# Kernel optimization log

Measured on AMD Instinct MI355X. Metric: run time of the kernel, lower is better.

Reference implementation:

```python
import jax, jax.numpy as jnp
import numpy as np

B, I, H, M, A, R, S, O = 256, 512, 1024, 128, 2048, 4, 3, 512
RS = R * M                      # read_size = num_heads * memory_content_size
P_READ = M + S + 3              # key + shift + (beta, gate, gamma) per read head
P = R * P_READ + (3 * M + S + 3)  # write head adds erase(M) + add(M)


def setup_inputs() -> dict:
    key = jax.random.key(0)
    ks = jax.random.split(key, 16)
    x = jax.random.normal(ks[0], (B, I), dtype=jnp.float32)
    h_prev = 0.1 * jax.random.normal(ks[1], (B, H), dtype=jnp.float32)
    c_prev = 0.1 * jax.random.normal(ks[2], (B, H), dtype=jnp.float32)
    read_w_prev = jax.nn.softmax(jax.random.normal(ks[3], (B, R, A)), axis=-1)
    write_w_prev = jax.nn.softmax(jax.random.normal(ks[4], (B, A)), axis=-1)
    # init_state uses normal(mean=0.5, std=0.2) for memory
    memory_prev = 0.5 + 0.2 * jax.random.normal(ks[5], (B, M, A), dtype=jnp.float32)
    read_vec_prev = 0.1 * jax.random.normal(ks[6], (B, RS), dtype=jnp.float32)
    sc = 0.02
    Wx = sc * jax.random.normal(ks[7], (I + RS, 4 * H), dtype=jnp.float32)
    Wh = sc * jax.random.normal(ks[8], (H, 4 * H), dtype=jnp.float32)
    b_lstm = jnp.zeros((4 * H,), dtype=jnp.float32)
    Wo_h = sc * jax.random.normal(ks[9], (H, O), dtype=jnp.float32)
    bo_h = jnp.zeros((O,), dtype=jnp.float32)
    Wint = sc * jax.random.normal(ks[10], (H, P), dtype=jnp.float32)
    b_int = jnp.zeros((P,), dtype=jnp.float32)
    Wout = sc * jax.random.normal(ks[11], (RS, O), dtype=jnp.float32)
    b_out = jnp.zeros((O,), dtype=jnp.float32)
    return dict(x=x, h_prev=h_prev, c_prev=c_prev, read_w_prev=read_w_prev,
                write_w_prev=write_w_prev, memory_prev=memory_prev,
                read_vec_prev=read_vec_prev, Wx=Wx, Wh=Wh, b_lstm=b_lstm,
                Wo_h=Wo_h, bo_h=bo_h, Wint=Wint, b_int=b_int, Wout=Wout, b_out=b_out)


def _address(k, beta, g, s, gamma, w_prev, mem):
    """NTM/DNC addressing: cosine content sim -> softmax -> gate -> circular shift -> sharpen.
    k: [B,Rh,M], beta/g/gamma: [B,Rh], s: [B,Rh,S], w_prev: [B,Rh,A], mem: [B,M,A] -> w: [B,Rh,A]"""
    eps = 1e-8
    kn = jnp.linalg.norm(k, axis=-1, keepdims=True)          # [B,Rh,1]
    mn = jnp.linalg.norm(mem, axis=1)                        # [B,A]
    sim = jnp.einsum('brm,bma->bra', k, mem) / (kn * mn[:, None, :] + eps)
    w_c = jax.nn.softmax(beta[..., None] * sim, axis=-1)
    w_g = g[..., None] * w_c + (1.0 - g[..., None]) * w_prev
    # circular convolution over S shift offsets centered at 0
    rolled = jnp.stack([jnp.roll(w_g, off, axis=-1) for off in range(-(S // 2), S // 2 + 1)], axis=-1)  # [B,Rh,A,S]
    w_s = jnp.einsum('bras,brs->bra', rolled, s)
    w_pow = (w_s + 1e-12) ** gamma[..., None]
    return w_pow / (jnp.sum(w_pow, axis=-1, keepdims=True) + eps)


def reference(x, h_prev, c_prev, read_w_prev, write_w_prev, memory_prev, read_vec_prev,
              Wx, Wh, b_lstm, Wo_h, bo_h, Wint, b_int, Wout, b_out):
    b = x.shape[0]
    # ---- controller (LSTM over [input, prev read vector]) ----
    z = jnp.concatenate([x, read_vec_prev], axis=-1) @ Wx + h_prev @ Wh + b_lstm
    i_g, f_g, g_g, o_g = jnp.split(z, 4, axis=-1)
    c = jax.nn.sigmoid(f_g) * c_prev + jax.nn.sigmoid(i_g) * jnp.tanh(g_g)
    h = jax.nn.sigmoid(o_g) * jnp.tanh(c)
    output_from_hidden = h @ Wo_h + bo_h
    p = h @ Wint + b_int                                    # interface update_data
    # ---- read heads ----
    pr = p[:, :R * P_READ].reshape(b, R, P_READ)
    k_r = pr[..., :M]
    beta_r = jax.nn.softplus(pr[..., M])
    g_r = jax.nn.sigmoid(pr[..., M + 1])
    gamma_r = 1.0 + jax.nn.softplus(pr[..., M + 2])
    s_r = jax.nn.softmax(pr[..., M + 3:], axis=-1)
    w_read = _address(k_r, beta_r, g_r, s_r, gamma_r, read_w_prev, memory_prev)
    # ---- write head ----
    pw = p[:, R * P_READ:]
    k_w = pw[:, :M]
    beta_w = jax.nn.softplus(pw[:, M])
    g_w = jax.nn.sigmoid(pw[:, M + 1])
    gamma_w = 1.0 + jax.nn.softplus(pw[:, M + 2])
    s_w = jax.nn.softmax(pw[:, M + 3:M + 3 + S], axis=-1)
    erase = jax.nn.sigmoid(pw[:, M + 3 + S:2 * M + 3 + S])
    add = pw[:, 2 * M + 3 + S:]
    w_write = _address(k_w[:, None], beta_w[:, None], g_w[:, None], s_w[:, None],
                       gamma_w[:, None], write_w_prev[:, None], memory_prev)[:, 0]
    # ---- read from PREVIOUS memory (as in DNCCell.forward) ----
    read_vec = jnp.einsum('bma,bra->brm', memory_prev, w_read).reshape(b, RS)
    # ---- erase/add memory edit ----
    memory_new = memory_prev * (1.0 - jnp.einsum('bm,ba->bma', erase, w_write)) \
               + jnp.einsum('bm,ba->bma', add, w_write)
    final_output = output_from_hidden + read_vec @ Wout + b_out
    return final_output, memory_new
```

## Files before the change

kernel.cpp:

```cpp
#include <hip/hip_runtime.h>
#include <math.h>

#define B_ 256
#define I_ 512
#define H_ 1024
#define M_ 128
#define A_ 2048
#define R_ 4
#define S_ 3
#define O_ 512
#define RS_ 512
#define P_ 926
#define PW_OFF 536
#define NP_ 1438
#define SK_ 4

typedef unsigned short ushort_t;
typedef __attribute__((ext_vector_type(8))) short bf16x8;
typedef __attribute__((ext_vector_type(4))) float f32x4;
typedef __attribute__((ext_vector_type(4))) unsigned short u16x4;

__device__ __forceinline__ float sigmoidf_(float x) { return 1.0f / (1.0f + expf(-x)); }
__device__ __forceinline__ float softplusf_(float x) {
    return (x > 20.0f) ? x : log1pf(expf(x));
}
__device__ __forceinline__ ushort_t f2bf(float f) {
    unsigned int u = __float_as_uint(f);
    u = (u + 0x7FFFu + ((u >> 16) & 1u)) >> 16;
    return (ushort_t)u;
}

__device__ __forceinline__ float pval(const float* __restrict__ pp,
                                      const float* __restrict__ b_int,
                                      int b, int col) {
    size_t o = (size_t)b * NP_ + col;
    size_t st = (size_t)B_ * NP_;
    return b_int[col] + pp[o] + pp[o + st] + pp[o + 2 * st] + pp[o + 3 * st];
}

__device__ __forceinline__ float block_sum_(float v, float* red) {
    #pragma unroll
    for (int off = 32; off; off >>= 1) v += __shfl_down(v, off, 64);
    __syncthreads();
    if ((threadIdx.x & 63) == 0) red[threadIdx.x >> 6] = v;
    __syncthreads();
    return red[0] + red[1] + red[2] + red[3];
}
__device__ __forceinline__ float block_max_(float v, float* red) {
    #pragma unroll
    for (int off = 32; off; off >>= 1) v = fmaxf(v, __shfl_down(v, off, 64));
    __syncthreads();
    if ((threadIdx.x & 63) == 0) red[threadIdx.x >> 6] = v;
    __syncthreads();
    return fmaxf(fmaxf(red[0], red[1]), fmaxf(red[2], red[3]));
}

__device__ __forceinline__ void transpose_tile(
    const float* __restrict__ W, ushort_t* __restrict__ WT,
    int K, int N, int ostride, int koff, int bx, int by, float (*tile)[33])
{
    int k0 = by * 32, n0 = bx * 32;
    int tx = threadIdx.x & 31, ty = threadIdx.x >> 5;
    #pragma unroll
    for (int i = 0; i < 4; ++i) {
        int k = ty + i * 8;
        int n = n0 + tx;
        float v = (n < N) ? W[(size_t)(k0 + k) * N + n] : 0.0f;
        tile[tx][k] = v;
    }
    __syncthreads();
    #pragma unroll
    for (int i = 0; i < 4; ++i) {
        int nl = ty + i * 8;
        int n = n0 + nl;
        if (n < N) WT[(size_t)n * ostride + koff + k0 + tx] = f2bf(tile[nl][tx]);
    }
}

__global__ __launch_bounds__(256) void setup_kernel(
    const float* __restrict__ x, const float* __restrict__ rv,
    const float* __restrict__ hp,
    const float* __restrict__ Wx, const float* __restrict__ Wh,
    const float* __restrict__ Wint, const float* __restrict__ Wo_h,
    const float* __restrict__ Wout,
    ushort_t* __restrict__ xin, ushort_t* __restrict__ WxhT,
    ushort_t* __restrict__ WpT, ushort_t* __restrict__ WoutT)
{
    __shared__ float tile[32][33];
    int r = blockIdx.x;
    if (r < 4096) { transpose_tile(Wx, WxhT, 1024, 4096, 2048, 0,    r % 128, r / 128, tile); return; }
    r -= 4096;
    if (r < 4096) { transpose_tile(Wh, WxhT, 1024, 4096, 2048, 1024, r % 128, r / 128, tile); return; }
    r -= 4096;
    if (r < 928)  { transpose_tile(Wint, WpT, 1024, 926, 1024, 0,    r % 29,  r / 29,  tile); return; }
    r -= 928;
    if (r < 512)  { transpose_tile(Wo_h, WpT + (size_t)926 * 1024, 1024, 512, 1024, 0, r % 16, r / 16, tile); return; }
    r -= 512;
    if (r < 256)  { transpose_tile(Wout, WoutT, 512, 512, 512, 0,    r % 16,  r / 16,  tile); return; }
    r -= 256;
    int idx = r * 256 + threadIdx.x;
    int b = idx >> 11, j = idx & 2047;
    float v;
    if (j < 512)       v = x[b * 512 + j];
    else if (j < 1024) v = rv[b * 512 + (j - 512)];
    else               v = hp[b * 1024 + (j - 1024)];
    xin[idx] = f2bf(v);
}

template<bool NALIGN>
__global__ __launch_bounds__(256) void gemm_bf16_k(
    const ushort_t* __restrict__ A, int lda,
    const ushort_t* __restrict__ BT, int ldb,
    float* __restrict__ Cpart,
    int N, int Ks)
{
    __shared__ ushort_t As[64][40];
    __shared__ ushort_t Bs[64][40];
    int tid = threadIdx.x;
    int bm0 = blockIdx.y * 64, bn0 = blockIdx.x * 64;
    int kbeg = blockIdx.z * Ks, kend = kbeg + Ks;
    int srow = tid >> 2;
    int scol = (tid & 3) << 3;
    int wv = tid >> 6, l = tid & 63;
    int wm = (wv & 1) * 32, wn = (wv >> 1) * 32;
    int lane16 = l & 15, quad = l >> 4;

    f32x4 z4 = {0.0f, 0.0f, 0.0f, 0.0f};
    f32x4 acc00 = z4, acc01 = z4, acc10 = z4, acc11 = z4;

    const ushort_t* ap = A + (size_t)(bm0 + srow) * lda + scol;
    bool bvalid = NALIGN || (bn0 + srow) < N;
    const ushort_t* bp = BT + (size_t)(bn0 + srow) * ldb + scol;
    float4 fz = {0.0f, 0.0f, 0.0f, 0.0f};

    for (int k0 = kbeg; k0 < kend; k0 += 32) {
        *(float4*)&As[srow][scol] = *(const float4*)(ap + k0);
        if (bvalid) *(float4*)&Bs[srow][scol] = *(const float4*)(bp + k0);
        else        *(float4*)&Bs[srow][scol] = fz;
        __syncthreads();
        bf16x8 a0 = *(const bf16x8*)&As[wm + lane16][quad * 8];
        bf16x8 a1 = *(const bf16x8*)&As[wm + 16 + lane16][quad * 8];
        bf16x8 b0 = *(const bf16x8*)&Bs[wn + lane16][quad * 8];
        bf16x8 b1 = *(const bf16x8*)&Bs[wn + 16 + lane16][quad * 8];
        acc00 = __builtin_amdgcn_mfma_f32_16x16x32_bf16(a0, b0, acc00, 0, 0, 0);
        acc01 = __builtin_amdgcn_mfma_f32_16x16x32_bf16(a0, b1, acc01, 0, 0, 0);
        acc10 = __builtin_amdgcn_mfma_f32_16x16x32_bf16(a1, b0, acc10, 0, 0, 0);
        acc11 = __builtin_amdgcn_mfma_f32_16x16x32_bf16(a1, b1, acc11, 0, 0, 0);
        __syncthreads();
    }

    float* C = Cpart + (size_t)blockIdx.z * gridDim.y * 64 * N;
    #pragma unroll
    for (int gi = 0; gi < 2; ++gi) {
        #pragma unroll
        for (int gj = 0; gj < 2; ++gj) {
            const f32x4& acc = gi == 0 ? (gj == 0 ? acc00 : acc01)
                                       : (gj == 0 ? acc10 : acc11);
            int col = bn0 + wn + gj * 16 + lane16;
            if (NALIGN || col < N) {
                #pragma unroll
                for (int r2 = 0; r2 < 4; ++r2) {
                    int row = bm0 + wm + gi * 16 + quad * 4 + r2;
                    C[(size_t)row * N + col] = acc[r2];
                }
            }
        }
    }
}

__global__ __launch_bounds__(256) void gates_kernel(
    const float* __restrict__ zpart, const float* __restrict__ b_lstm,
    const float* __restrict__ c_prev, ushort_t* __restrict__ h)
{
    int g = blockIdx.x * 256 + threadIdx.x;
    int b = g >> 8, j = (g & 255) << 2;
    size_t st = (size_t)B_ * 4096;
    size_t zb = (size_t)b * 4096 + j;
    f32x4 zs[4];
    #pragma unroll
    for (int q = 0; q < 4; ++q) {
        size_t o = zb + q * 1024;
        f32x4 v = *(const f32x4*)(zpart + o);
        v += *(const f32x4*)(zpart + o + st);
        v += *(const f32x4*)(zpart + o + 2 * st);
        v += *(const f32x4*)(zpart + o + 3 * st);
        v += *(const f32x4*)(b_lstm + q * 1024 + j);
        zs[q] = v;
    }
    f32x4 cp = *(const f32x4*)(c_prev + (size_t)b * 1024 + j);
    u16x4 hv;
    #pragma unroll
    for (int e = 0; e < 4; ++e) {
        float c = sigmoidf_(zs[1][e]) * cp[e] + sigmoidf_(zs[0][e]) * tanhf(zs[2][e]);
        hv[e] = f2bf(sigmoidf_(zs[3][e]) * tanhf(c));
    }
    *(u16x4*)(h + (size_t)b * 1024 + j) = hv;
}

__global__ __launch_bounds__(256) void sim_kernel(
    const float* __restrict__ mem, const float* __restrict__ pohpart,
    const float* __restrict__ b_int,
    float* __restrict__ dots,
    float* __restrict__ mn)
{
    int b = blockIdx.y;
    int a = blockIdx.x * 256 + threadIdx.x;
    __shared__ float ks[5][M_];
    for (int idx = threadIdx.x; idx < 5 * M_; idx += 256) {
        int h = idx >> 7, m = idx & 127;
        int col = (h < 4) ? h * 134 + m : PW_OFF + m;
        ks[h][m] = pval(pohpart, b_int, b, col);
    }
    __syncthreads();
    const float* mb = mem + (size_t)b * M_ * A_ + a;
    float d0 = 0, d1 = 0, d2 = 0, d3 = 0, d4 = 0, nn = 0;
    #pragma unroll 8
    for (int m = 0; m < M_; ++m) {
        float v = mb[(size_t)m * A_];
        d0 += v * ks[0][m]; d1 += v * ks[1][m]; d2 += v * ks[2][m];
        d3 += v * ks[3][m]; d4 += v * ks[4][m];
        nn += v * v;
    }
    size_t base = (size_t)b * 5 * A_ + a;
    dots[base + 0 * A_] = d0; dots[base + 1 * A_] = d1; dots[base + 2 * A_] = d2;
    dots[base + 3 * A_] = d3; dots[base + 4 * A_] = d4;
    mn[(size_t)b * A_ + a] = sqrtf(nn);
}

__global__ __launch_bounds__(256) void address_kernel(
    const float* __restrict__ pohpart, const float* __restrict__ b_int,
    const float* __restrict__ dots, const float* __restrict__ mn,
    const float* __restrict__ read_w_prev, const float* __restrict__ write_w_prev,
    float* __restrict__ w_read, float* __restrict__ w_write)
{
    int head = blockIdx.x;
    int b = blockIdx.y;
    int t = threadIdx.x;
    __shared__ float wg[A_];
    __shared__ float red[4];

    int pb = (head < 4) ? head * 134 : PW_OFF;
    float beta  = softplusf_(pval(pohpart, b_int, b, pb + 128));
    float g     = sigmoidf_(pval(pohpart, b_int, b, pb + 129));
    float gamma = 1.0f + softplusf_(pval(pohpart, b_int, b, pb + 130));
    float e0 = pval(pohpart, b_int, b, pb + 131);
    float e1 = pval(pohpart, b_int, b, pb + 132);
    float e2 = pval(pohpart, b_int, b, pb + 133);
    float smax = fmaxf(e0, fmaxf(e1, e2));
    float x0 = __expf(e0 - smax), x1 = __expf(e1 - smax), x2 = __expf(e2 - smax);
    float sden = x0 + x1 + x2;
    float s0 = x0 / sden, s1 = x1 / sden, s2 = x2 / sden;

    float kacc = 0.0f;
    if (t < M_) { float kv = pval(pohpart, b_int, b, pb + t); kacc = kv * kv; }
    float kn = sqrtf(block_sum_(kacc, red));

    const float* db = dots + ((size_t)b * 5 + head) * A_;
    const float* mb = mn + (size_t)b * A_;
    float logit[8];
    float lmax = -1e30f;
    #pragma unroll
    for (int i = 0; i < 8; ++i) {
        int a = t + 256 * i;
        float sim = db[a] / (kn * mb[a] + 1e-8f);
        logit[i] = beta * sim;
        lmax = fmaxf(lmax, logit[i]);
    }
    lmax = block_max_(lmax, red);
    float ex[8]; float lsum = 0.0f;
    #pragma unroll
    for (int i = 0; i < 8; ++i) { ex[i] = __expf(logit[i] - lmax); lsum += ex[i]; }
    lsum = block_sum_(lsum, red);
    float inv_lsum = 1.0f / lsum;

    const float* wprev = (head < 4) ? read_w_prev + ((size_t)b * 4 + head) * A_
                                    : write_w_prev + (size_t)b * A_;
    #pragma unroll
    for (int i = 0; i < 8; ++i) {
        int a = t + 256 * i;
        wg[a] = g * (ex[i] * inv_lsum) + (1.0f - g) * wprev[a];
    }
    __syncthreads();
    float wpow[8]; float psum = 0.0f;
    #pragma unroll
    for (int i = 0; i < 8; ++i) {
        int a = t + 256 * i;
        float ws = s0 * wg[(a + 1) & (A_ - 1)] + s1 * wg[a] + s2 * wg[(a + A_ - 1) & (A_ - 1)];
        float wp2 = __expf(gamma * __logf(ws + 1e-12f));
        wpow[i] = wp2; psum += wp2;
    }
    psum = block_sum_(psum, red);
    float inv = 1.0f / (psum + 1e-8f);
    float* wout = (head < 4) ? w_read + ((size_t)b * 4 + head) * A_
                             : w_write + (size_t)b * A_;
    #pragma unroll
    for (int i = 0; i < 8; ++i) wout[t + 256 * i] = wpow[i] * inv;
}

__global__ __launch_bounds__(256) void update_kernel(
    const float* __restrict__ mem, const float* __restrict__ pohpart,
    const float* __restrict__ b_int,
    const float* __restrict__ w_read, const float* __restrict__ w_write,
    float* __restrict__ mem_new,
    ushort_t* __restrict__ read_vec)
{
    int bm = blockIdx.x;
    int b = bm >> 7, m = bm & 127;
    int t = threadIdx.x;
    int wv = t >> 6, l = t & 63;
    float er = sigmoidf_(pval(pohpart, b_int, b, 670 + m));
    float ad = pval(pohpart, b_int, b, 798 + m);
    const f32x4* m4  = (const f32x4*)(mem + ((size_t)b * M_ + m) * A_);
    const f32x4* ww4 = (const f32x4*)(w_write + (size_t)b * A_);
    const f32x4* wr4 = (const f32x4*)(w_read + (size_t)b * 4 * A_);
    f32x4* o4 = (f32x4*)(mem_new + ((size_t)b * M_ + m) * A_);
    float s[4] = {0, 0, 0, 0};
    #pragma unroll
    for (int j = 0; j < 2; ++j) {
        int a4 = wv * 128 + l + 64 * j;
        f32x4 v = m4[a4], w = ww4[a4];
        f32x4 r0 = wr4[a4], r1 = wr4[512 + a4], r2 = wr4[1024 + a4], r3 = wr4[1536 + a4];
        f32x4 ov;
        #pragma unroll
        for (int c = 0; c < 4; ++c) {
            ov[c] = v[c] * (1.0f - er * w[c]) + ad * w[c];
            s[0] += v[c] * r0[c];
            s[1] += v[c] * r1[c];
            s[2] += v[c] * r2[c];
            s[3] += v[c] * r3[c];
        }
        o4[a4] = ov;
    }
    __shared__ float part[4][4];
    #pragma unroll
    for (int r = 0; r < 4; ++r) {
        float v = s[r];
        #pragma unroll
        for (int off = 32; off; off >>= 1) v += __shfl_down(v, off, 64);
        if (l == 0) part[wv][r] = v;
    }
    __syncthreads();
    if (t < 4) {
        float sum = part[0][t] + part[1][t] + part[2][t] + part[3][t];
        read_vec[(size_t)b * RS_ + t * M_ + m] = f2bf(sum);
    }
}

__global__ __launch_bounds__(256) void gemm_final_k(
    const ushort_t* __restrict__ A,
    const ushort_t* __restrict__ BT,
    const float* __restrict__ pohpart,
    const float* __restrict__ bo_h, const float* __restrict__ b_out,
    float* __restrict__ C)
{
    __shared__ ushort_t As[64][40];
    __shared__ ushort_t Bs[64][40];
    int tid = threadIdx.x;
    int bm0 = blockIdx.y * 64, bn0 = blockIdx.x * 64;
    int srow = tid >> 2, scol = (tid & 3) << 3;
    int wv = tid >> 6, l = tid & 63;
    int wm = (wv & 1) * 32, wn = (wv >> 1) * 32;
    int lane16 = l & 15, quad = l >> 4;

    f32x4 z4 = {0.0f, 0.0f, 0.0f, 0.0f};
    f32x4 acc00 = z4, acc01 = z4, acc10 = z4, acc11 = z4;
    const ushort_t* ap = A + (size_t)(bm0 + srow) * 512 + scol;
    const ushort_t* bp = BT + (size_t)(bn0 + srow) * 512 + scol;

    for (int k0 = 0; k0 < 512; k0 += 32) {
        *(float4*)&As[srow][scol] = *(const float4*)(ap + k0);
        *(float4*)&Bs[srow][scol] = *(const float4*)(bp + k0);
        __syncthreads();
        bf16x8 a0 = *(const bf16x8*)&As[wm + lane16][quad * 8];
        bf16x8 a1 = *(const bf16x8*)&As[wm + 16 + lane16][quad * 8];
        bf16x8 b0 = *(const bf16x8*)&Bs[wn + lane16][quad * 8];
        bf16x8 b1 = *(const bf16x8*)&Bs[wn + 16 + lane16][quad * 8];
        acc00 = __builtin_amdgcn_mfma_f32_16x16x32_bf16(a0, b0, acc00, 0, 0, 0);
        acc01 = __builtin_amdgcn_mfma_f32_16x16x32_bf16(a0, b1, acc01, 0, 0, 0);
        acc10 = __builtin_amdgcn_mfma_f32_16x16x32_bf16(a1, b0, acc10, 0, 0, 0);
        acc11 = __builtin_amdgcn_mfma_f32_16x16x32_bf16(a1, b1, acc11, 0, 0, 0);
        __syncthreads();
    }

    size_t st = (size_t)B_ * NP_;
    #pragma unroll
    for (int gi = 0; gi < 2; ++gi) {
        #pragma unroll
        for (int gj = 0; gj < 2; ++gj) {
            const f32x4& acc = gi == 0 ? (gj == 0 ? acc00 : acc01)
                                       : (gj == 0 ? acc10 : acc11);
            int col = bn0 + wn + gj * 16 + lane16;
            float badd = bo_h[col] + b_out[col];
            #pragma unroll
            for (int r2 = 0; r2 < 4; ++r2) {
                int row = bm0 + wm + gi * 16 + quad * 4 + r2;
                size_t o = (size_t)row * NP_ + 926 + col;
                float oh = pohpart[o] + pohpart[o + st] + pohpart[o + 2 * st] + pohpart[o + 3 * st];
                C[(size_t)row * 512 + col] = acc[r2] + badd + oh;
            }
        }
    }
}

extern "C" void kernel_launch(void* const* d_in, const int* in_sizes, int n_in,
                              void* d_out, int out_size, void* d_ws, size_t ws_size,
                              hipStream_t stream) {
    (void)in_sizes; (void)n_in; (void)out_size; (void)ws_size;
    const float* x            = (const float*)d_in[0];
    const float* h_prev       = (const float*)d_in[1];
    const float* c_prev       = (const float*)d_in[2];
    const float* read_w_prev  = (const float*)d_in[3];
    const float* write_w_prev = (const float*)d_in[4];
    const float* memory_prev  = (const float*)d_in[5];
    const float* read_vec_prev= (const float*)d_in[6];
    const float* Wx           = (const float*)d_in[7];
    const float* Wh           = (const float*)d_in[8];
    const float* b_lstm       = (const float*)d_in[9];
    const float* Wo_h         = (const float*)d_in[10];
    const float* bo_h         = (const float*)d_in[11];
    const float* Wint         = (const float*)d_in[12];
    const float* b_int        = (const float*)d_in[13];
    const float* Wout         = (const float*)d_in[14];
    const float* b_out        = (const float*)d_in[15];
    float* out = (float*)d_out;
    float* mem_new_out = out + (size_t)B_ * O_;

    char* wsp = (char*)d_ws;
    ushort_t* xin_bf = (ushort_t*)wsp; wsp += (size_t)B_ * 2048 * 2;
    ushort_t* h_bf   = (ushort_t*)wsp; wsp += (size_t)B_ * H_ * 2;
    ushort_t* rv_bf  = (ushort_t*)wsp; wsp += (size_t)B_ * RS_ * 2;
    ushort_t* WxhT   = (ushort_t*)wsp; wsp += (size_t)4096 * 2048 * 2;
    ushort_t* WpT    = (ushort_t*)wsp; wsp += (size_t)NP_ * 1024 * 2;
    ushort_t* WoutT  = (ushort_t*)wsp; wsp += (size_t)512 * 512 * 2;
    float* zpart     = (float*)wsp;    wsp += (size_t)SK_ * B_ * 4096 * 4;
    float* pohpart   = (float*)wsp;    wsp += (size_t)SK_ * B_ * NP_ * 4;
    float* dots      = (float*)wsp;    wsp += (size_t)B_ * 5 * A_ * 4;
    float* mn        = (float*)wsp;    wsp += (size_t)B_ * A_ * 4;
    float* w_read    = (float*)wsp;    wsp += (size_t)B_ * R_ * A_ * 4;
    float* w_write   = (float*)wsp;    wsp += (size_t)B_ * A_ * 4;

    setup_kernel<<<dim3(4096 + 4096 + 928 + 512 + 256 + 2048), 256, 0, stream>>>(
        x, read_vec_prev, h_prev, Wx, Wh, Wint, Wo_h, Wout,
        xin_bf, WxhT, WpT, WoutT);
    gemm_bf16_k<true><<<dim3(4096 / 64, B_ / 64, SK_), 256, 0, stream>>>(
        xin_bf, 2048, WxhT, 2048, zpart, 4096, 2048 / SK_);
    gates_kernel<<<dim3(B_ * H_ / 1024), 256, 0, stream>>>(zpart, b_lstm, c_prev, h_bf);
    gemm_bf16_k<false><<<dim3(23, B_ / 64, SK_), 256, 0, stream>>>(
        h_bf, 1024, WpT, 1024, pohpart, NP_, 1024 / SK_);
    sim_kernel<<<dim3(A_ / 256, B_), 256, 0, stream>>>(memory_prev, pohpart, b_int, dots, mn);
    address_kernel<<<dim3(5, B_), 256, 0, stream>>>(
        pohpart, b_int, dots, mn, read_w_prev, write_w_prev, w_read, w_write);
    update_kernel<<<dim3(B_ * M_), 256, 0, stream>>>(
        memory_prev, pohpart, b_int, w_read, w_write, mem_new_out, rv_bf);
    gemm_final_k<<<dim3(O_ / 64, B_ / 64), 256, 0, stream>>>(
        rv_bf, WoutT, pohpart, bo_h, b_out, out);
}
```

Measured before the change: 670.9 us.

## Vectorize sim/address kernels and retile memory update to reuse addressing weights

The sim kernel now has each thread handle four adjacent memory columns with float4 loads, and it launches four times fewer blocks. The address kernel switches to float4 loads and stores in a contiguous layout. The update kernel is retiled so each block covers 8 memory rows by half the columns, loading the read and write weights once per block instead of once per row. Read-vector partials are written in fp32 per half and summed and converted to bf16 inside the final GEMM's A-tile load, reusing the xin_bf workspace for the partials. The aims are fewer redundant weight reads and wider memory transactions, at the cost of fewer blocks for the sim kernel and more registers per thread.

```diff
diff --git a/kernel.cpp b/kernel.cpp
--- a/kernel.cpp
+++ b/kernel.cpp
@@ -204,7 +204,7 @@
     float* __restrict__ mn)
 {
     int b = blockIdx.y;
-    int a = blockIdx.x * 256 + threadIdx.x;
+    int a = (blockIdx.x * 256 + threadIdx.x) * 4;
     __shared__ float ks[5][M_];
     for (int idx = threadIdx.x; idx < 5 * M_; idx += 256) {
         int h = idx >> 7, m = idx & 127;
@@ -213,18 +213,43 @@
     }
     __syncthreads();
     const float* mb = mem + (size_t)b * M_ * A_ + a;
-    float d0 = 0, d1 = 0, d2 = 0, d3 = 0, d4 = 0, nn = 0;
-    #pragma unroll 8
-    for (int m = 0; m < M_; ++m) {
-        float v = mb[(size_t)m * A_];
-        d0 += v * ks[0][m]; d1 += v * ks[1][m]; d2 += v * ks[2][m];
-        d3 += v * ks[3][m]; d4 += v * ks[4][m];
-        nn += v * v;
+    f32x4 z = {0.0f, 0.0f, 0.0f, 0.0f};
+    f32x4 d0 = z, d1 = z, d2 = z, d3 = z, d4 = z, nn = z;
+    #pragma unroll 2
+    for (int m = 0; m < M_; m += 4) {
+        f32x4 vv[4];
+        #pragma unroll
+        for (int mm = 0; mm < 4; ++mm)
+            vv[mm] = *(const f32x4*)(mb + (size_t)(m + mm) * A_);
+        f32x4 k0 = *(const f32x4*)&ks[0][m];
+        f32x4 k1 = *(const f32x4*)&ks[1][m];
+        f32x4 k2 = *(const f32x4*)&ks[2][m];
+        f32x4 k3 = *(const f32x4*)&ks[3][m];
+        f32x4 k4 = *(const f32x4*)&ks[4][m];
+        #pragma unroll
+        for (int mm = 0; mm < 4; ++mm) {
+            #pragma unroll
+            for (int c = 0; c < 4; ++c) {
+                float v = vv[mm][c];
+                d0[c] += v * k0[mm];
+                d1[c] += v * k1[mm];
+                d2[c] += v * k2[mm];
+                d3[c] += v * k3[mm];
+                d4[c] += v * k4[mm];
+                nn[c] += v * v;
+            }
+        }
     }
     size_t base = (size_t)b * 5 * A_ + a;
-    dots[base + 0 * A_] = d0; dots[base + 1 * A_] = d1; dots[base + 2 * A_] = d2;
-    dots[base + 3 * A_] = d3; dots[base + 4 * A_] = d4;
-    mn[(size_t)b * A_ + a] = sqrtf(nn);
+    *(f32x4*)(dots + base + 0 * A_) = d0;
+    *(f32x4*)(dots + base + 1 * A_) = d1;
+    *(f32x4*)(dots + base + 2 * A_) = d2;
+    *(f32x4*)(dots + base + 3 * A_) = d3;
+    *(f32x4*)(dots + base + 4 * A_) = d4;
+    f32x4 rt;
+    #pragma unroll
+    for (int c = 0; c < 4; ++c) rt[c] = sqrtf(nn[c]);
+    *(f32x4*)(mn + (size_t)b * A_ + a) = rt;
 }
 
 __global__ __launch_bounds__(256) void address_kernel(
@@ -257,44 +282,63 @@
 
     const float* db = dots + ((size_t)b * 5 + head) * A_;
     const float* mb = mn + (size_t)b * A_;
-    float logit[8];
+    f32x4 dA = *(const f32x4*)(db + 4 * t);
+    f32x4 dB = *(const f32x4*)(db + 1024 + 4 * t);
+    f32x4 mA = *(const f32x4*)(mb + 4 * t);
+    f32x4 mB = *(const f32x4*)(mb + 1024 + 4 * t);
+    f32x4 lA, lB;
     float lmax = -1e30f;
     #pragma unroll
-    for (int i = 0; i < 8; ++i) {
-        int a = t + 256 * i;
-        float sim = db[a] / (kn * mb[a] + 1e-8f);
-        logit[i] = beta * sim;
-        lmax = fmaxf(lmax, logit[i]);
+    for (int c = 0; c < 4; ++c) {
+        lA[c] = beta * dA[c] / (kn * mA[c] + 1e-8f);
+        lB[c] = beta * dB[c] / (kn * mB[c] + 1e-8f);
+        lmax = fmaxf(lmax, fmaxf(lA[c], lB[c]));
     }
     lmax = block_max_(lmax, red);
-    float ex[8]; float lsum = 0.0f;
-    #pragma unroll
-    for (int i = 0; i < 8; ++i) { ex[i] = __expf(logit[i] - lmax); lsum += ex[i]; }
+    f32x4 eA, eB;
+    float lsum = 0.0f;
+    #pragma unroll
+    for (int c = 0; c < 4; ++c) {
+        eA[c] = __expf(lA[c] - lmax);
+        eB[c] = __expf(lB[c] - lmax);
+        lsum += eA[c] + eB[c];
+    }
     lsum = block_sum_(lsum, red);
     float inv_lsum = 1.0f / lsum;
 
     const float* wprev = (head < 4) ? read_w_prev + ((size_t)b * 4 + head) * A_
                                     : write_w_prev + (size_t)b * A_;
-    #pragma unroll
-    for (int i = 0; i < 8; ++i) {
-        int a = t + 256 * i;
-        wg[a] = g * (ex[i] * inv_lsum) + (1.0f - g) * wprev[a];
-    }
-    __syncthreads();
-    float wpow[8]; float psum = 0.0f;
-    #pragma unroll
-    for (int i = 0; i < 8; ++i) {
-        int a = t + 256 * i;
+    f32x4 pA = *(const f32x4*)(wprev + 4 * t);
+    f32x4 pB = *(const f32x4*)(wprev + 1024 + 4 * t);
+    f32x4 gA, gB;
+    #pragma unroll
+    for (int c = 0; c < 4; ++c) {
+        gA[c] = g * (eA[c] * inv_lsum) + (1.0f - g) * pA[c];
+        gB[c] = g * (eB[c] * inv_lsum) + (1.0f - g) * pB[c];
+    }
+    *(f32x4*)&wg[4 * t] = gA;
+    *(f32x4*)&wg[1024 + 4 * t] = gB;
+    __syncthreads();
+    f32x4 wA, wB;
+    float psum = 0.0f;
+    #pragma unroll
+    for (int c = 0; c < 4; ++c) {
+        int a = 4 * t + c;
         float ws = s0 * wg[(a + 1) & (A_ - 1)] + s1 * wg[a] + s2 * wg[(a + A_ - 1) & (A_ - 1)];
-        float wp2 = __expf(gamma * __logf(ws + 1e-12f));
-        wpow[i] = wp2; psum += wp2;
+        wA[c] = __expf(gamma * __logf(ws + 1e-12f));
+        a = 1024 + 4 * t + c;
+        ws = s0 * wg[(a + 1) & (A_ - 1)] + s1 * wg[a] + s2 * wg[(a + A_ - 1) & (A_ - 1)];
+        wB[c] = __expf(gamma * __logf(ws + 1e-12f));
+        psum += wA[c] + wB[c];
     }
     psum = block_sum_(psum, red);
     float inv = 1.0f / (psum + 1e-8f);
+    #pragma unroll
+    for (int c = 0; c < 4; ++c) { wA[c] *= inv; wB[c] *= inv; }
     float* wout = (head < 4) ? w_read + ((size_t)b * 4 + head) * A_
                              : w_write + (size_t)b * A_;
-    #pragma unroll
-    for (int i = 0; i < 8; ++i) wout[t + 256 * i] = wpow[i] * inv;
+    *(f32x4*)(wout + 4 * t) = wA;
+    *(f32x4*)(wout + 1024 + 4 * t) = wB;
 }
 
 __global__ __launch_bounds__(256) void update_kernel(
@@ -302,52 +346,71 @@
     const float* __restrict__ b_int,
     const float* __restrict__ w_read, const float* __restrict__ w_write,
     float* __restrict__ mem_new,
-    ushort_t* __restrict__ read_vec)
-{
-    int bm = blockIdx.x;
-    int b = bm >> 7, m = bm & 127;
+    float* __restrict__ rv_part)
+{
+    int blk = blockIdx.x;
+    int b = blk >> 5;
+    int half = (blk >> 4) & 1;
+    int m0 = (blk & 15) << 3;
     int t = threadIdx.x;
     int wv = t >> 6, l = t & 63;
-    float er = sigmoidf_(pval(pohpart, b_int, b, 670 + m));
-    float ad = pval(pohpart, b_int, b, 798 + m);
-    const f32x4* m4  = (const f32x4*)(mem + ((size_t)b * M_ + m) * A_);
-    const f32x4* ww4 = (const f32x4*)(w_write + (size_t)b * A_);
-    const f32x4* wr4 = (const f32x4*)(w_read + (size_t)b * 4 * A_);
-    f32x4* o4 = (f32x4*)(mem_new + ((size_t)b * M_ + m) * A_);
-    float s[4] = {0, 0, 0, 0};
-    #pragma unroll
-    for (int j = 0; j < 2; ++j) {
-        int a4 = wv * 128 + l + 64 * j;
-        f32x4 v = m4[a4], w = ww4[a4];
-        f32x4 r0 = wr4[a4], r1 = wr4[512 + a4], r2 = wr4[1024 + a4], r3 = wr4[1536 + a4];
+    __shared__ float ser[8], sad[8];
+    __shared__ float spart[4][8][4];
+    if (t < 8)       ser[t] = sigmoidf_(pval(pohpart, b_int, b, 670 + m0 + t));
+    else if (t < 16) sad[t - 8] = pval(pohpart, b_int, b, 798 + m0 + (t - 8));
+
+    int col = half * 1024 + t * 4;
+    const float* wrb = w_read + (size_t)b * 4 * A_ + col;
+    f32x4 ww  = *(const f32x4*)(w_write + (size_t)b * A_ + col);
+    f32x4 wr0 = *(const f32x4*)(wrb);
+    f32x4 wr1 = *(const f32x4*)(wrb + A_);
+    f32x4 wr2 = *(const f32x4*)(wrb + 2 * A_);
+    f32x4 wr3 = *(const f32x4*)(wrb + 3 * A_);
+    __syncthreads();
+
+    float acc[8][4];
+    #pragma unroll
+    for (int mi = 0; mi < 8; ++mi)
+        acc[mi][0] = acc[mi][1] = acc[mi][2] = acc[mi][3] = 0.0f;
+
+    const float* mrow = mem + ((size_t)b * M_ + m0) * A_ + col;
+    float* orow = mem_new + ((size_t)b * M_ + m0) * A_ + col;
+    #pragma unroll
+    for (int mi = 0; mi < 8; ++mi) {
+        f32x4 v = *(const f32x4*)(mrow + (size_t)mi * A_);
+        float er = ser[mi], ad = sad[mi];
         f32x4 ov;
         #pragma unroll
         for (int c = 0; c < 4; ++c) {
-            ov[c] = v[c] * (1.0f - er * w[c]) + ad * w[c];
-            s[0] += v[c] * r0[c];
-            s[1] += v[c] * r1[c];
-            s[2] += v[c] * r2[c];
-            s[3] += v[c] * r3[c];
+            ov[c] = v[c] * (1.0f - er * ww[c]) + ad * ww[c];
+            acc[mi][0] += v[c] * wr0[c];
+            acc[mi][1] += v[c] * wr1[c];
+            acc[mi][2] += v[c] * wr2[c];
+            acc[mi][3] += v[c] * wr3[c];
         }
-        o4[a4] = ov;
-    }
-    __shared__ float part[4][4];
-    #pragma unroll
-    for (int r = 0; r < 4; ++r) {
-        float v = s[r];
-        #pragma unroll
-        for (int off = 32; off; off >>= 1) v += __shfl_down(v, off, 64);
-        if (l == 0) part[wv][r] = v;
-    }
-    __syncthreads();
-    if (t < 4) {
-        float sum = part[0][t] + part[1][t] + part[2][t] + part[3][t];
-        read_vec[(size_t)b * RS_ + t * M_ + m] = f2bf(sum);
+        *(f32x4*)(orow + (size_t)mi * A_) = ov;
+    }
+
+    #pragma unroll
+    for (int mi = 0; mi < 8; ++mi) {
+        #pragma unroll
+        for (int h = 0; h < 4; ++h) {
+            float v = acc[mi][h];
+            #pragma unroll
+            for (int off = 32; off; off >>= 1) v += __shfl_down(v, off, 64);
+            if (l == 0) spart[wv][mi][h] = v;
+        }
+    }
+    __syncthreads();
+    if (t < 32) {
+        int mi = t >> 2, h = t & 3;
+        float s = spart[0][mi][h] + spart[1][mi][h] + spart[2][mi][h] + spart[3][mi][h];
+        rv_part[((size_t)half * B_ + b) * RS_ + h * M_ + m0 + mi] = s;
     }
 }
 
 __global__ __launch_bounds__(256) void gemm_final_k(
-    const ushort_t* __restrict__ A,
+    const float* __restrict__ rv_part,
     const ushort_t* __restrict__ BT,
     const float* __restrict__ pohpart,
     const float* __restrict__ bo_h, const float* __restrict__ b_out,
@@ -364,11 +427,18 @@
 
     f32x4 z4 = {0.0f, 0.0f, 0.0f, 0.0f};
     f32x4 acc00 = z4, acc01 = z4, acc10 = z4, acc11 = z4;
-    const ushort_t* ap = A + (size_t)(bm0 + srow) * 512 + scol;
+    const float* rp0 = rv_part + (size_t)(bm0 + srow) * RS_ + scol;
+    const float* rp1 = rp0 + (size_t)B_ * RS_;
     const ushort_t* bp = BT + (size_t)(bn0 + srow) * 512 + scol;
 
     for (int k0 = 0; k0 < 512; k0 += 32) {
-        *(float4*)&As[srow][scol] = *(const float4*)(ap + k0);
+        f32x4 u0 = *(const f32x4*)(rp0 + k0) + *(const f32x4*)(rp1 + k0);
+        f32x4 u1 = *(const f32x4*)(rp0 + k0 + 4) + *(const f32x4*)(rp1 + k0 + 4);
+        u16x4 w0, w1;
+        #pragma unroll
+        for (int c = 0; c < 4; ++c) { w0[c] = f2bf(u0[c]); w1[c] = f2bf(u1[c]); }
+        *(u16x4*)&As[srow][scol] = w0;
+        *(u16x4*)&As[srow][scol + 4] = w1;
         *(float4*)&Bs[srow][scol] = *(const float4*)(bp + k0);
         __syncthreads();
         bf16x8 a0 = *(const bf16x8*)&As[wm + lane16][quad * 8];
@@ -428,7 +498,6 @@
     char* wsp = (char*)d_ws;
     ushort_t* xin_bf = (ushort_t*)wsp; wsp += (size_t)B_ * 2048 * 2;
     ushort_t* h_bf   = (ushort_t*)wsp; wsp += (size_t)B_ * H_ * 2;
-    ushort_t* rv_bf  = (ushort_t*)wsp; wsp += (size_t)B_ * RS_ * 2;
     ushort_t* WxhT   = (ushort_t*)wsp; wsp += (size_t)4096 * 2048 * 2;
     ushort_t* WpT    = (ushort_t*)wsp; wsp += (size_t)NP_ * 1024 * 2;
     ushort_t* WoutT  = (ushort_t*)wsp; wsp += (size_t)512 * 512 * 2;
@@ -438,6 +507,7 @@
     float* mn        = (float*)wsp;    wsp += (size_t)B_ * A_ * 4;
     float* w_read    = (float*)wsp;    wsp += (size_t)B_ * R_ * A_ * 4;
     float* w_write   = (float*)wsp;    wsp += (size_t)B_ * A_ * 4;
+    float* rv_part   = (float*)xin_bf;
 
     setup_kernel<<<dim3(4096 + 4096 + 928 + 512 + 256 + 2048), 256, 0, stream>>>(
         x, read_vec_prev, h_prev, Wx, Wh, Wint, Wo_h, Wout,
@@ -447,11 +517,11 @@
     gates_kernel<<<dim3(B_ * H_ / 1024), 256, 0, stream>>>(zpart, b_lstm, c_prev, h_bf);
     gemm_bf16_k<false><<<dim3(23, B_ / 64, SK_), 256, 0, stream>>>(
         h_bf, 1024, WpT, 1024, pohpart, NP_, 1024 / SK_);
-    sim_kernel<<<dim3(A_ / 256, B_), 256, 0, stream>>>(memory_prev, pohpart, b_int, dots, mn);
+    sim_kernel<<<dim3(A_ / 1024, B_), 256, 0, stream>>>(memory_prev, pohpart, b_int, dots, mn);
     address_kernel<<<dim3(5, B_), 256, 0, stream>>>(
         pohpart, b_int, dots, mn, read_w_prev, write_w_prev, w_read, w_write);
-    update_kernel<<<dim3(B_ * M_), 256, 0, stream>>>(
-        memory_prev, pohpart, b_int, w_read, w_write, mem_new_out, rv_bf);
+    update_kernel<<<dim3(B_ * 32), 256, 0, stream>>>(
+        memory_prev, pohpart, b_int, w_read, w_write, mem_new_out, rv_part);
     gemm_final_k<<<dim3(O_ / 64, B_ / 64), 256, 0, stream>>>(
-        rv_bf, WoutT, pohpart, bo_h, b_out, out);
-}
+        rv_part, WoutT, pohpart, bo_h, b_out, out);
+}
```

Result: faster. 635.3 us (-5.3%).

## Fuse similarity, addressing, memory update and output GEMM into one per-batch kernel

Applied to the files above, without the earlier changes.

Replaces the sim, address, update and final GEMM kernels with a single kernel that runs one 512-thread block per batch element. Similarity dots, addressing weights and the read vector stay in shared memory, and the output projection becomes an fp32 FMA loop reading Wout directly, so the Wout transpose is dropped. This removes the dots, mn and weight round-trips through global memory plus three launches. In exchange only 256 blocks are launched, memory is read twice per block, and LDS use is large, which may limit occupancy.

```diff
diff --git a/kernel.cpp b/kernel.cpp
--- a/kernel.cpp
+++ b/kernel.cpp
@@ -38,21 +38,23 @@
     return b_int[col] + pp[o] + pp[o + st] + pp[o + 2 * st] + pp[o + 3 * st];
 }
 
-__device__ __forceinline__ float block_sum_(float v, float* red) {
+__device__ __forceinline__ float bsum8(float v, float* red, int wv, int l) {
     #pragma unroll
     for (int off = 32; off; off >>= 1) v += __shfl_down(v, off, 64);
     __syncthreads();
-    if ((threadIdx.x & 63) == 0) red[threadIdx.x >> 6] = v;
-    __syncthreads();
-    return red[0] + red[1] + red[2] + red[3];
-}
-__device__ __forceinline__ float block_max_(float v, float* red) {
+    if (l == 0) red[wv] = v;
+    __syncthreads();
+    return red[0] + red[1] + red[2] + red[3] + red[4] + red[5] + red[6] + red[7];
+}
+__device__ __forceinline__ float bmax8(float v, float* red, int wv, int l) {
     #pragma unroll
     for (int off = 32; off; off >>= 1) v = fmaxf(v, __shfl_down(v, off, 64));
     __syncthreads();
-    if ((threadIdx.x & 63) == 0) red[threadIdx.x >> 6] = v;
-    __syncthreads();
-    return fmaxf(fmaxf(red[0], red[1]), fmaxf(red[2], red[3]));
+    if (l == 0) red[wv] = v;
+    __syncthreads();
+    float m0 = fmaxf(fmaxf(red[0], red[1]), fmaxf(red[2], red[3]));
+    float m1 = fmaxf(fmaxf(red[4], red[5]), fmaxf(red[6], red[7]));
+    return fmaxf(m0, m1);
 }
 
 __device__ __forceinline__ void transpose_tile(
@@ -82,9 +84,8 @@
     const float* __restrict__ hp,
     const float* __restrict__ Wx, const float* __restrict__ Wh,
     const float* __restrict__ Wint, const float* __restrict__ Wo_h,
-    const float* __restrict__ Wout,
     ushort_t* __restrict__ xin, ushort_t* __restrict__ WxhT,
-    ushort_t* __restrict__ WpT, ushort_t* __restrict__ WoutT)
+    ushort_t* __restrict__ WpT)
 {
     __shared__ float tile[32][33];
     int r = blockIdx.x;
@@ -96,8 +97,6 @@
     r -= 928;
     if (r < 512)  { transpose_tile(Wo_h, WpT + (size_t)926 * 1024, 1024, 512, 1024, 0, r % 16, r / 16, tile); return; }
     r -= 512;
-    if (r < 256)  { transpose_tile(Wout, WoutT, 512, 512, 512, 0,    r % 16,  r / 16,  tile); return; }
-    r -= 256;
     int idx = r * 256 + threadIdx.x;
     int b = idx >> 11, j = idx & 2047;
     float v;
@@ -197,208 +196,203 @@
     *(u16x4*)(h + (size_t)b * 1024 + j) = hv;
 }
 
-__global__ __launch_bounds__(256) void sim_kernel(
+__global__ __launch_bounds__(512) void mega_kernel(
     const float* __restrict__ mem, const float* __restrict__ pohpart,
     const float* __restrict__ b_int,
-    float* __restrict__ dots,
-    float* __restrict__ mn)
+    const float* __restrict__ read_w_prev, const float* __restrict__ write_w_prev,
+    const float* __restrict__ Wout, const float* __restrict__ bo_h,
+    const float* __restrict__ b_out,
+    float* __restrict__ out,
+    float* __restrict__ mem_new)
 {
-    int b = blockIdx.y;
-    int a = blockIdx.x * 256 + threadIdx.x;
+    int b = blockIdx.x;
+    int t = threadIdx.x;
+    int wv = t >> 6, l = t & 63;
+
+    __shared__ float dw[5][A_];
+    __shared__ float wg[A_];
     __shared__ float ks[5][M_];
-    for (int idx = threadIdx.x; idx < 5 * M_; idx += 256) {
+    __shared__ float rvp[M_][8][4];
+    __shared__ float red[8];
+
+    for (int idx = t; idx < 5 * M_; idx += 512) {
         int h = idx >> 7, m = idx & 127;
         int col = (h < 4) ? h * 134 + m : PW_OFF + m;
         ks[h][m] = pval(pohpart, b_int, b, col);
     }
     __syncthreads();
-    const float* mb = mem + (size_t)b * M_ * A_ + a;
-    float d0 = 0, d1 = 0, d2 = 0, d3 = 0, d4 = 0, nn = 0;
-    #pragma unroll 8
-    for (int m = 0; m < M_; ++m) {
-        float v = mb[(size_t)m * A_];
-        d0 += v * ks[0][m]; d1 += v * ks[1][m]; d2 += v * ks[2][m];
-        d3 += v * ks[3][m]; d4 += v * ks[4][m];
-        nn += v * v;
-    }
-    size_t base = (size_t)b * 5 * A_ + a;
-    dots[base + 0 * A_] = d0; dots[base + 1 * A_] = d1; dots[base + 2 * A_] = d2;
-    dots[base + 3 * A_] = d3; dots[base + 4 * A_] = d4;
-    mn[(size_t)b * A_ + a] = sqrtf(nn);
-}
-
-__global__ __launch_bounds__(256) void address_kernel(
-    const float* __restrict__ pohpart, const float* __restrict__ b_int,
-    const float* __restrict__ dots, const float* __restrict__ mn,
-    const float* __restrict__ read_w_prev, const float* __restrict__ write_w_prev,
-    float* __restrict__ w_read, float* __restrict__ w_write)
-{
-    int head = blockIdx.x;
-    int b = blockIdx.y;
-    int t = threadIdx.x;
-    __shared__ float wg[A_];
-    __shared__ float red[4];
-
-    int pb = (head < 4) ? head * 134 : PW_OFF;
-    float beta  = softplusf_(pval(pohpart, b_int, b, pb + 128));
-    float g     = sigmoidf_(pval(pohpart, b_int, b, pb + 129));
-    float gamma = 1.0f + softplusf_(pval(pohpart, b_int, b, pb + 130));
-    float e0 = pval(pohpart, b_int, b, pb + 131);
-    float e1 = pval(pohpart, b_int, b, pb + 132);
-    float e2 = pval(pohpart, b_int, b, pb + 133);
-    float smax = fmaxf(e0, fmaxf(e1, e2));
-    float x0 = __expf(e0 - smax), x1 = __expf(e1 - smax), x2 = __expf(e2 - smax);
-    float sden = x0 + x1 + x2;
-    float s0 = x0 / sden, s1 = x1 / sden, s2 = x2 / sden;
-
-    float kacc = 0.0f;
-    if (t < M_) { float kv = pval(pohpart, b_int, b, pb + t); kacc = kv * kv; }
-    float kn = sqrtf(block_sum_(kacc, red));
-
-    const float* db = dots + ((size_t)b * 5 + head) * A_;
-    const float* mb = mn + (size_t)b * A_;
-    float logit[8];
-    float lmax = -1e30f;
-    #pragma unroll
-    for (int i = 0; i < 8; ++i) {
-        int a = t + 256 * i;
-        float sim = db[a] / (kn * mb[a] + 1e-8f);
-        logit[i] = beta * sim;
-        lmax = fmaxf(lmax, logit[i]);
-    }
-    lmax = block_max_(lmax, red);
-    float ex[8]; float lsum = 0.0f;
-    #pragma unroll
-    for (int i = 0; i < 8; ++i) { ex[i] = __expf(logit[i] - lmax); lsum += ex[i]; }
-    lsum = block_sum_(lsum, red);
-    float inv_lsum = 1.0f / lsum;
-
-    const float* wprev = (head < 4) ? read_w_prev + ((size_t)b * 4 + head) * A_
-                                    : write_w_prev + (size_t)b * A_;
-    #pragma unroll
-    for (int i = 0; i < 8; ++i) {
-        int a = t + 256 * i;
-        wg[a] = g * (ex[i] * inv_lsum) + (1.0f - g) * wprev[a];
-    }
-    __syncthreads();
-    float wpow[8]; float psum = 0.0f;
-    #pragma unroll
-    for (int i = 0; i < 8; ++i) {
-        int a = t + 256 * i;
-        float ws = s0 * wg[(a + 1) & (A_ - 1)] + s1 * wg[a] + s2 * wg[(a + A_ - 1) & (A_ - 1)];
-        float wp2 = __expf(gamma * __logf(ws + 1e-12f));
-        wpow[i] = wp2; psum += wp2;
-    }
-    psum = block_sum_(psum, red);
-    float inv = 1.0f / (psum + 1e-8f);
-    float* wout = (head < 4) ? w_read + ((size_t)b * 4 + head) * A_
-                             : w_write + (size_t)b * A_;
-    #pragma unroll
-    for (int i = 0; i < 8; ++i) wout[t + 256 * i] = wpow[i] * inv;
-}
-
-__global__ __launch_bounds__(256) void update_kernel(
-    const float* __restrict__ mem, const float* __restrict__ pohpart,
-    const float* __restrict__ b_int,
-    const float* __restrict__ w_read, const float* __restrict__ w_write,
-    float* __restrict__ mem_new,
-    ushort_t* __restrict__ read_vec)
-{
-    int bm = blockIdx.x;
-    int b = bm >> 7, m = bm & 127;
-    int t = threadIdx.x;
-    int wv = t >> 6, l = t & 63;
-    float er = sigmoidf_(pval(pohpart, b_int, b, 670 + m));
-    float ad = pval(pohpart, b_int, b, 798 + m);
-    const f32x4* m4  = (const f32x4*)(mem + ((size_t)b * M_ + m) * A_);
-    const f32x4* ww4 = (const f32x4*)(w_write + (size_t)b * A_);
-    const f32x4* wr4 = (const f32x4*)(w_read + (size_t)b * 4 * A_);
-    f32x4* o4 = (f32x4*)(mem_new + ((size_t)b * M_ + m) * A_);
-    float s[4] = {0, 0, 0, 0};
-    #pragma unroll
-    for (int j = 0; j < 2; ++j) {
-        int a4 = wv * 128 + l + 64 * j;
-        f32x4 v = m4[a4], w = ww4[a4];
-        f32x4 r0 = wr4[a4], r1 = wr4[512 + a4], r2 = wr4[1024 + a4], r3 = wr4[1536 + a4];
-        f32x4 ov;
+
+    const float* mb = mem + (size_t)b * M_ * A_ + 4 * t;
+    f32x4 z = {0.0f, 0.0f, 0.0f, 0.0f};
+    f32x4 d0 = z, d1 = z, d2 = z, d3 = z, d4 = z, nn = z;
+    #pragma unroll 2
+    for (int m = 0; m < M_; m += 4) {
+        f32x4 vv[4];
+        #pragma unroll
+        for (int mm = 0; mm < 4; ++mm)
+            vv[mm] = *(const f32x4*)(mb + (size_t)(m + mm) * A_);
+        #pragma unroll
+        for (int mm = 0; mm < 4; ++mm) {
+            float k0 = ks[0][m + mm], k1 = ks[1][m + mm], k2 = ks[2][m + mm];
+            float k3 = ks[3][m + mm], k4 = ks[4][m + mm];
+            #pragma unroll
+            for (int c = 0; c < 4; ++c) {
+                float v = vv[mm][c];
+                d0[c] += v * k0; d1[c] += v * k1; d2[c] += v * k2;
+                d3[c] += v * k3; d4[c] += v * k4;
+                nn[c] += v * v;
+            }
+        }
+    }
+    *(f32x4*)&dw[0][4 * t] = d0;
+    *(f32x4*)&dw[1][4 * t] = d1;
+    *(f32x4*)&dw[2][4 * t] = d2;
+    *(f32x4*)&dw[3][4 * t] = d3;
+    *(f32x4*)&dw[4][4 * t] = d4;
+    f32x4 rt;
+    #pragma unroll
+    for (int c = 0; c < 4; ++c) rt[c] = sqrtf(nn[c]);
+
+    for (int head = 0; head < 5; ++head) {
+        int pb = (head < 4) ? head * 134 : PW_OFF;
+        float beta  = softplusf_(pval(pohpart, b_int, b, pb + 128));
+        float g     = sigmoidf_(pval(pohpart, b_int, b, pb + 129));
+        float gamma = 1.0f + softplusf_(pval(pohpart, b_int, b, pb + 130));
+        float e0 = pval(pohpart, b_int, b, pb + 131);
+        float e1 = pval(pohpart, b_int, b, pb + 132);
+        float e2 = pval(pohpart, b_int, b, pb + 133);
+        float smax = fmaxf(e0, fmaxf(e1, e2));
+        float x0 = __expf(e0 - smax), x1 = __expf(e1 - smax), x2 = __expf(e2 - smax);
+        float sden = x0 + x1 + x2;
+        float s0 = x0 / sden, s1 = x1 / sden, s2 = x2 / sden;
+
+        float kacc = (t < M_) ? ks[head][t] * ks[head][t] : 0.0f;
+        float kn = sqrtf(bsum8(kacc, red, wv, l));
+
+        f32x4 dd = *(const f32x4*)&dw[head][4 * t];
+        f32x4 lg;
+        float lmax = -1e30f;
         #pragma unroll
         for (int c = 0; c < 4; ++c) {
-            ov[c] = v[c] * (1.0f - er * w[c]) + ad * w[c];
-            s[0] += v[c] * r0[c];
-            s[1] += v[c] * r1[c];
-            s[2] += v[c] * r2[c];
-            s[3] += v[c] * r3[c];
-        }
-        o4[a4] = ov;
-    }
-    __shared__ float part[4][4];
-    #pragma unroll
-    for (int r = 0; r < 4; ++r) {
-        float v = s[r];
-        #pragma unroll
-        for (int off = 32; off; off >>= 1) v += __shfl_down(v, off, 64);
-        if (l == 0) part[wv][r] = v;
-    }
-    __syncthreads();
-    if (t < 4) {
-        float sum = part[0][t] + part[1][t] + part[2][t] + part[3][t];
-        read_vec[(size_t)b * RS_ + t * M_ + m] = f2bf(sum);
-    }
-}
-
-__global__ __launch_bounds__(256) void gemm_final_k(
-    const ushort_t* __restrict__ A,
-    const ushort_t* __restrict__ BT,
-    const float* __restrict__ pohpart,
-    const float* __restrict__ bo_h, const float* __restrict__ b_out,
-    float* __restrict__ C)
-{
-    __shared__ ushort_t As[64][40];
-    __shared__ ushort_t Bs[64][40];
-    int tid = threadIdx.x;
-    int bm0 = blockIdx.y * 64, bn0 = blockIdx.x * 64;
-    int srow = tid >> 2, scol = (tid & 3) << 3;
-    int wv = tid >> 6, l = tid & 63;
-    int wm = (wv & 1) * 32, wn = (wv >> 1) * 32;
-    int lane16 = l & 15, quad = l >> 4;
-
-    f32x4 z4 = {0.0f, 0.0f, 0.0f, 0.0f};
-    f32x4 acc00 = z4, acc01 = z4, acc10 = z4, acc11 = z4;
-    const ushort_t* ap = A + (size_t)(bm0 + srow) * 512 + scol;
-    const ushort_t* bp = BT + (size_t)(bn0 + srow) * 512 + scol;
-
-    for (int k0 = 0; k0 < 512; k0 += 32) {
-        *(float4*)&As[srow][scol] = *(const float4*)(ap + k0);
-        *(float4*)&Bs[srow][scol] = *(const float4*)(bp + k0);
+            lg[c] = beta * dd[c] / (kn * rt[c] + 1e-8f);
+            lmax = fmaxf(lmax, lg[c]);
+        }
+        lmax = bmax8(lmax, red, wv, l);
+        f32x4 ex;
+        float lsum = 0.0f;
+        #pragma unroll
+        for (int c = 0; c < 4; ++c) { ex[c] = __expf(lg[c] - lmax); lsum += ex[c]; }
+        lsum = bsum8(lsum, red, wv, l);
+        float inv_lsum = 1.0f / lsum;
+
+        const float* wprev = (head < 4) ? read_w_prev + ((size_t)b * 4 + head) * A_
+                                        : write_w_prev + (size_t)b * A_;
+        f32x4 pv = *(const f32x4*)(wprev + 4 * t);
+        f32x4 gv;
+        #pragma unroll
+        for (int c = 0; c < 4; ++c)
+            gv[c] = g * (ex[c] * inv_lsum) + (1.0f - g) * pv[c];
+        *(f32x4*)&wg[4 * t] = gv;
         __syncthreads();
-        bf16x8 a0 = *(const bf16x8*)&As[wm + lane16][quad * 8];
-        bf16x8 a1 = *(const bf16x8*)&As[wm + 16 + lane16][quad * 8];
-        bf16x8 b0 = *(const bf16x8*)&Bs[wn + lane16][quad * 8];
-        bf16x8 b1 = *(const bf16x8*)&Bs[wn + 16 + lane16][quad * 8];
-        acc00 = __builtin_amdgcn_mfma_f32_16x16x32_bf16(a0, b0, acc00, 0, 0, 0);
-        acc01 = __builtin_amdgcn_mfma_f32_16x16x32_bf16(a0, b1, acc01, 0, 0, 0);
-        acc10 = __builtin_amdgcn_mfma_f32_16x16x32_bf16(a1, b0, acc10, 0, 0, 0);
-        acc11 = __builtin_amdgcn_mfma_f32_16x16x32_bf16(a1, b1, acc11, 0, 0, 0);
+        f32x4 wp;
+        float psum = 0.0f;
+        #pragma unroll
+        for (int c = 0; c < 4; ++c) {
+            int a = 4 * t + c;
+            float ws = s0 * wg[(a + 1) & (A_ - 1)] + s1 * wg[a] + s2 * wg[(a + A_ - 1) & (A_ - 1)];
+            wp[c] = __expf(gamma * __logf(ws + 1e-12f));
+            psum += wp[c];
+        }
+        psum = bsum8(psum, red, wv, l);
+        float inv = 1.0f / (psum + 1e-8f);
+        #pragma unroll
+        for (int c = 0; c < 4; ++c) wp[c] *= inv;
+        *(f32x4*)&dw[head][4 * t] = wp;
         __syncthreads();
     }
 
-    size_t st = (size_t)B_ * NP_;
-    #pragma unroll
-    for (int gi = 0; gi < 2; ++gi) {
-        #pragma unroll
-        for (int gj = 0; gj < 2; ++gj) {
-            const f32x4& acc = gi == 0 ? (gj == 0 ? acc00 : acc01)
-                                       : (gj == 0 ? acc10 : acc11);
-            int col = bn0 + wn + gj * 16 + lane16;
-            float badd = bo_h[col] + b_out[col];
+    float* er_s = &ks[0][0];
+    float* ad_s = &ks[1][0];
+    if (t < M_)            er_s[t] = sigmoidf_(pval(pohpart, b_int, b, 670 + t));
+    else if (t < 2 * M_)   ad_s[t - M_] = pval(pohpart, b_int, b, 798 + (t - M_));
+    __syncthreads();
+
+    f32x4 ww = *(const f32x4*)&dw[4][4 * t];
+    f32x4 w0 = *(const f32x4*)&dw[0][4 * t];
+    f32x4 w1 = *(const f32x4*)&dw[1][4 * t];
+    f32x4 w2 = *(const f32x4*)&dw[2][4 * t];
+    f32x4 w3 = *(const f32x4*)&dw[3][4 * t];
+    const float* mrow = mem + (size_t)b * M_ * A_ + 4 * t;
+    float* orow = mem_new + (size_t)b * M_ * A_ + 4 * t;
+    #pragma unroll 1
+    for (int m0v = 0; m0v < M_; m0v += 4) {
+        f32x4 vv[4];
+        #pragma unroll
+        for (int mm = 0; mm < 4; ++mm)
+            vv[mm] = *(const f32x4*)(mrow + (size_t)(m0v + mm) * A_);
+        #pragma unroll
+        for (int mm = 0; mm < 4; ++mm) {
+            float er = er_s[m0v + mm], ad = ad_s[m0v + mm];
+            f32x4 ov;
+            float a0 = 0, a1 = 0, a2 = 0, a3 = 0;
             #pragma unroll
-            for (int r2 = 0; r2 < 4; ++r2) {
-                int row = bm0 + wm + gi * 16 + quad * 4 + r2;
-                size_t o = (size_t)row * NP_ + 926 + col;
-                float oh = pohpart[o] + pohpart[o + st] + pohpart[o + 2 * st] + pohpart[o + 3 * st];
-                C[(size_t)row * 512 + col] = acc[r2] + badd + oh;
+            for (int c = 0; c < 4; ++c) {
+                float v = vv[mm][c];
+                ov[c] = v * (1.0f - er * ww[c]) + ad * ww[c];
+                a0 += v * w0[c]; a1 += v * w1[c]; a2 += v * w2[c]; a3 += v * w3[c];
             }
-        }
+            *(f32x4*)(orow + (size_t)(m0v + mm) * A_) = ov;
+            float ah0 = a0, ah1 = a1, ah2 = a2, ah3 = a3;
+            #pragma unroll
+            for (int off = 32; off; off >>= 1) {
+                ah0 += __shfl_down(ah0, off, 64);
+                ah1 += __shfl_down(ah1, off, 64);
+                ah2 += __shfl_down(ah2, off, 64);
+                ah3 += __shfl_down(ah3, off, 64);
+            }
+            if (l == 0) {
+                rvp[m0v + mm][wv][0] = ah0;
+                rvp[m0v + mm][wv][1] = ah1;
+                rvp[m0v + mm][wv][2] = ah2;
+                rvp[m0v + mm][wv][3] = ah3;
+            }
+        }
+    }
+    __syncthreads();
+
+    float* rvs = wg;
+    {
+        int h = t >> 7, m = t & 127;
+        float s = 0.0f;
+        #pragma unroll
+        for (int w8 = 0; w8 < 8; ++w8) s += rvp[m][w8][h];
+        rvs[t] = s;
+    }
+    __syncthreads();
+
+    float* part = &rvp[0][0][0];
+    {
+        int q = t >> 7;
+        int oc = (t & 127) * 4;
+        f32x4 acc = {0.0f, 0.0f, 0.0f, 0.0f};
+        const float* wob = Wout + (size_t)q * M_ * O_ + oc;
+        #pragma unroll 4
+        for (int k = 0; k < M_; ++k) {
+            float rvk = rvs[q * M_ + k];
+            f32x4 wv4 = *(const f32x4*)(wob + (size_t)k * O_);
+            #pragma unroll
+            for (int c = 0; c < 4; ++c) acc[c] += rvk * wv4[c];
+        }
+        *(f32x4*)&part[q * 512 + oc] = acc;
+    }
+    __syncthreads();
+    {
+        int o = t;
+        size_t st = (size_t)B_ * NP_;
+        size_t po = (size_t)b * NP_ + 926 + o;
+        float oh = pohpart[po] + pohpart[po + st] + pohpart[po + 2 * st] + pohpart[po + 3 * st];
+        float s = part[o] + part[512 + o] + part[1024 + o] + part[1536 + o];
+        out[(size_t)b * O_ + o] = s + oh + bo_h[o] + b_out[o];
     }
 }
 
@@ -428,30 +422,20 @@
     char* wsp = (char*)d_ws;
     ushort_t* xin_bf = (ushort_t*)wsp; wsp += (size_t)B_ * 2048 * 2;
     ushort_t* h_bf   = (ushort_t*)wsp; wsp += (size_t)B_ * H_ * 2;
-    ushort_t* rv_bf  = (ushort_t*)wsp; wsp += (size_t)B_ * RS_ * 2;
     ushort_t* WxhT   = (ushort_t*)wsp; wsp += (size_t)4096 * 2048 * 2;
     ushort_t* WpT    = (ushort_t*)wsp; wsp += (size_t)NP_ * 1024 * 2;
-    ushort_t* WoutT  = (ushort_t*)wsp; wsp += (size_t)512 * 512 * 2;
     float* zpart     = (float*)wsp;    wsp += (size_t)SK_ * B_ * 4096 * 4;
     float* pohpart   = (float*)wsp;    wsp += (size_t)SK_ * B_ * NP_ * 4;
-    float* dots      = (float*)wsp;    wsp += (size_t)B_ * 5 * A_ * 4;
-    float* mn        = (float*)wsp;    wsp += (size_t)B_ * A_ * 4;
-    float* w_read    = (float*)wsp;    wsp += (size_t)B_ * R_ * A_ * 4;
-    float* w_write   = (float*)wsp;    wsp += (size_t)B_ * A_ * 4;
-
-    setup_kernel<<<dim3(4096 + 4096 + 928 + 512 + 256 + 2048), 256, 0, stream>>>(
-        x, read_vec_prev, h_prev, Wx, Wh, Wint, Wo_h, Wout,
-        xin_bf, WxhT, WpT, WoutT);
+
+    setup_kernel<<<dim3(4096 + 4096 + 928 + 512 + 2048), 256, 0, stream>>>(
+        x, read_vec_prev, h_prev, Wx, Wh, Wint, Wo_h,
+        xin_bf, WxhT, WpT);
     gemm_bf16_k<true><<<dim3(4096 / 64, B_ / 64, SK_), 256, 0, stream>>>(
         xin_bf, 2048, WxhT, 2048, zpart, 4096, 2048 / SK_);
     gates_kernel<<<dim3(B_ * H_ / 1024), 256, 0, stream>>>(zpart, b_lstm, c_prev, h_bf);
     gemm_bf16_k<false><<<dim3(23, B_ / 64, SK_), 256, 0, stream>>>(
         h_bf, 1024, WpT, 1024, pohpart, NP_, 1024 / SK_);
-    sim_kernel<<<dim3(A_ / 256, B_), 256, 0, stream>>>(memory_prev, pohpart, b_int, dots, mn);
-    address_kernel<<<dim3(5, B_), 256, 0, stream>>>(
-        pohpart, b_int, dots, mn, read_w_prev, write_w_prev, w_read, w_write);
-    update_kernel<<<dim3(B_ * M_), 256, 0, stream>>>(
-        memory_prev, pohpart, b_int, w_read, w_write, mem_new_out, rv_bf);
-    gemm_final_k<<<dim3(O_ / 64, B_ / 64), 256, 0, stream>>>(
-        rv_bf, WoutT, pohpart, bo_h, b_out, out);
-}
+    mega_kernel<<<dim3(B_), 512, 0, stream>>>(
+        memory_prev, pohpart, b_int, read_w_prev, write_w_prev,
+        Wout, bo_h, b_out, out, mem_new_out);
+}
```

After: 614.6 us. 1.09x faster.
